# Kernel tuning notes

Measured on AMD Instinct MI355X. Metric: run time of the kernel, lower is better.

The kernel has to match this reference:

```python
import math
import jax, jax.numpy as jnp
import numpy as np

N, NFEAT, NHID, NCLASS, NLAYERS = 8192, 500, 128, 40, 4
ALPHA, GAMMA, LAMBDA, MAX_W = 0.1, 0.1, 0.5, 0.05


def _col_stochastic(w):
    # Uniform(0,1) -> clamp to [0, MAX_W] -> column normalize (ColumnStochasticGraphConvolution init)
    w = jnp.clip(w, 0.0, MAX_W)
    return w / jnp.clip(w.sum(axis=0, keepdims=True), 1e-8, None)


def setup_inputs() -> dict:
    key = jax.random.key(0)
    ks = jax.random.split(key, 10)
    x = jax.random.normal(ks[0], (N, NFEAT), dtype=jnp.float32)
    adj = (jax.random.uniform(ks[1], (N, N)) < 0.002).astype(jnp.float32)
    s_in = 1.0 / math.sqrt(NFEAT)
    fc_in_w = jax.random.uniform(ks[2], (NFEAT, NHID), minval=-s_in, maxval=s_in, dtype=jnp.float32)
    fc_in_b = jnp.zeros((NHID,), jnp.float32)
    c = jax.random.normal(ks[3], (NHID,), dtype=jnp.float32)
    s_h = 1.0 / math.sqrt(NHID)
    w_gcnii = jax.random.uniform(ks[4], (NLAYERS, NHID, NHID), minval=-s_h, maxval=s_h, dtype=jnp.float32)
    b_gcnii = jax.random.uniform(ks[5], (NLAYERS, NHID), minval=-s_h, maxval=s_h, dtype=jnp.float32)
    w_lin = jax.vmap(_col_stochastic)(jax.random.uniform(ks[6], (NLAYERS, NHID, NHID), dtype=jnp.float32))
    b_lin = jnp.zeros((NLAYERS, NHID), jnp.float32)
    fc_out_w = jax.random.uniform(ks[7], (NHID, NCLASS), minval=-s_h, maxval=s_h, dtype=jnp.float32)
    fc_out_b = jnp.zeros((NCLASS,), jnp.float32)
    return {"x": x, "adj": adj, "fc_in_w": fc_in_w, "fc_in_b": fc_in_b, "c": c,
            "w_gcnii": w_gcnii, "b_gcnii": b_gcnii, "w_lin": w_lin, "b_lin": b_lin,
            "fc_out_w": fc_out_w, "fc_out_b": fc_out_b}


def _normalize_adj(adj):
    # A_hat = D^{-1/2} (A + I) D^{-1/2}
    a = adj + jnp.eye(adj.shape[0], dtype=adj.dtype)
    deg = a.sum(axis=1)
    dinv = jnp.where(deg > 0, jax.lax.rsqrt(deg), 0.0)
    return dinv[:, None] * a * dinv[None, :]


def reference(x, adj, fc_in_w, fc_in_b, c, w_gcnii, b_gcnii, w_lin, b_lin, fc_out_w, fc_out_b):
    a_hat = _normalize_adj(adj)                      # [N, N]
    h = jax.nn.relu(x @ fc_in_w + fc_in_b)           # [N, nhid]
    h = (1.0 - GAMMA) * h + GAMMA * c[None, :]       # H0 preconditioning with learnable c
    h0 = h
    # dropout is identity in eval mode
    for i in range(NLAYERS):
        beta = math.log(LAMBDA / (i + 1) + 1.0)
        # linear propagation branch: A_hat @ (H W'_i) + b'_i  (column-stochastic W')
        linear_part = a_hat @ (h @ w_lin[i]) + b_lin[i]
        # GCNII branch: sigma(((1-a) A_hat H + a H0)((1-b) I + b W_i)) + b_i
        support = (1.0 - ALPHA) * (a_hat @ h) + ALPHA * h0
        gcnii = jax.nn.relu((1.0 - beta) * support + beta * (support @ w_gcnii[i]) + b_gcnii[i])
        h = linear_part + gcnii
    return h @ fc_out_w + fc_out_b                   # [N, nclass] logits
```

## Files before the change

### kernel.cpp

```cpp
#include <hip/hip_runtime.h>
#include <math.h>

#define NROWS 8192
#define NFEATD 500
#define NHID 128
#define NCLS 40
#define CAP 64
#define FCIN_BLOCKS (NROWS / 8)
#define CSR_BLOCKS  (NROWS / 4)

typedef float f32x4 __attribute__((ext_vector_type(4)));

__global__ __launch_bounds__(256) void k_pre(
    const float* __restrict__ x, const float* __restrict__ w,
    const float* __restrict__ b, const float* __restrict__ c,
    const float* __restrict__ adj,
    float* __restrict__ h, float* __restrict__ h0,
    float* __restrict__ dinv, int* __restrict__ cnts, int* __restrict__ cols)
{
    __shared__ float xs[8][504];
    int tid = threadIdx.x;
    if (blockIdx.x < FCIN_BLOCKS) {
        int col = tid & 127;
        int rg = tid >> 7;
        int r0 = blockIdx.x * 8;
        for (int rr = 0; rr < 8; ++rr)
            for (int k = tid; k < NFEATD; k += 256)
                xs[rr][k] = x[(size_t)(r0 + rr) * NFEATD + k];
        __syncthreads();
        float bias = b[col];
        float acc[4] = {bias, bias, bias, bias};
        for (int k4 = 0; k4 < NFEATD / 4; ++k4) {
            int k = k4 * 4;
            f32x4 a0 = *(const f32x4*)&xs[rg * 4 + 0][k];
            f32x4 a1 = *(const f32x4*)&xs[rg * 4 + 1][k];
            f32x4 a2 = *(const f32x4*)&xs[rg * 4 + 2][k];
            f32x4 a3 = *(const f32x4*)&xs[rg * 4 + 3][k];
            float w0 = w[(k + 0) * NHID + col];
            float w1 = w[(k + 1) * NHID + col];
            float w2 = w[(k + 2) * NHID + col];
            float w3 = w[(k + 3) * NHID + col];
            acc[0] += a0.x * w0 + a0.y * w1 + a0.z * w2 + a0.w * w3;
            acc[1] += a1.x * w0 + a1.y * w1 + a1.z * w2 + a1.w * w3;
            acc[2] += a2.x * w0 + a2.y * w1 + a2.z * w2 + a2.w * w3;
            acc[3] += a3.x * w0 + a3.y * w1 + a3.z * w2 + a3.w * w3;
        }
        float cv = c[col];
#pragma unroll
        for (int rr = 0; rr < 4; ++rr) {
            float hv = 0.9f * fmaxf(acc[rr], 0.0f) + 0.1f * cv;
            size_t o = (size_t)(r0 + rg * 4 + rr) * NHID + col;
            h[o] = hv;
            h0[o] = hv;
        }
    } else {
        int bid = blockIdx.x - FCIN_BLOCKS;
        int r = bid * 4 + (tid >> 6);
        int lane = tid & 63;
        const f32x4* row4 = (const f32x4*)(adj + (size_t)r * NROWS);
        int* mycols = cols + (size_t)r * CAP;
        unsigned long long lt = (1ull << lane) - 1ull;
        int cnt = 0;
        for (int it = 0; it < NROWS / 256; ++it) {
            f32x4 v = __builtin_nontemporal_load(&row4[it * 64 + lane]);
            int base = it * 256 + 4 * lane;
            bool nz; unsigned long long m;
            nz = (v.x != 0.0f); m = __ballot(nz);
            if (nz) { int p = cnt + __popcll(m & lt); mycols[p < CAP ? p : CAP - 1] = base; }
            cnt += __popcll(m);
            nz = (v.y != 0.0f); m = __ballot(nz);
            if (nz) { int p = cnt + __popcll(m & lt); mycols[p < CAP ? p : CAP - 1] = base + 1; }
            cnt += __popcll(m);
            nz = (v.z != 0.0f); m = __ballot(nz);
            if (nz) { int p = cnt + __popcll(m & lt); mycols[p < CAP ? p : CAP - 1] = base + 2; }
            cnt += __popcll(m);
            nz = (v.w != 0.0f); m = __ballot(nz);
            if (nz) { int p = cnt + __popcll(m & lt); mycols[p < CAP ? p : CAP - 1] = base + 3; }
            cnt += __popcll(m);
        }
        if (lane == 0) {
            cnts[r] = cnt < CAP ? cnt : CAP;
            dinv[r] = rsqrtf((float)cnt + 1.0f);
        }
    }
}

__global__ __launch_bounds__(256) void k_layer(
    const float* __restrict__ hin, const float* __restrict__ h0,
    const float* __restrict__ dinv, const int* __restrict__ cnts,
    const int* __restrict__ cols,
    const float* __restrict__ wlin, const float* __restrict__ blin,
    const float* __restrict__ wg, const float* __restrict__ bg,
    float beta, float* __restrict__ hout)
{
    __shared__ float ahs[8][NHID];
    __shared__ float ss[8][NHID];
    int tid = threadIdx.x;
    int lane = tid & 63;
    int wid = tid >> 6;
    int r0 = blockIdx.x * 8;

    for (int rr = 2 * wid; rr < 2 * wid + 2; ++rr) {
        int r = r0 + rr;
        int n = cnts[r];
        const int* mc = cols + (size_t)r * CAP;
        float ax = 0.f, ay = 0.f;
        int e = 0;
        for (; e + 4 <= n; e += 4) {
            int j0 = mc[e], j1 = mc[e + 1], j2 = mc[e + 2], j3 = mc[e + 3];
            float d0 = dinv[j0], d1 = dinv[j1], d2 = dinv[j2], d3 = dinv[j3];
            float2 v0 = ((const float2*)(hin + (size_t)j0 * NHID))[lane];
            float2 v1 = ((const float2*)(hin + (size_t)j1 * NHID))[lane];
            float2 v2 = ((const float2*)(hin + (size_t)j2 * NHID))[lane];
            float2 v3 = ((const float2*)(hin + (size_t)j3 * NHID))[lane];
            ax += d0 * v0.x + d1 * v1.x + d2 * v2.x + d3 * v3.x;
            ay += d0 * v0.y + d1 * v1.y + d2 * v2.y + d3 * v3.y;
        }
        for (; e < n; ++e) {
            int j = mc[e];
            float dj = dinv[j];
            float2 v = ((const float2*)(hin + (size_t)j * NHID))[lane];
            ax += dj * v.x;
            ay += dj * v.y;
        }
        float di = dinv[r];
        float2 vi = ((const float2*)(hin + (size_t)r * NHID))[lane];
        ax = di * (ax + di * vi.x);
        ay = di * (ay + di * vi.y);
        float2 h0v = ((const float2*)(h0 + (size_t)r * NHID))[lane];
        ((float2*)&ahs[rr][0])[lane] = make_float2(ax, ay);
        ((float2*)&ss[rr][0])[lane] =
            make_float2(0.9f * ax + 0.1f * h0v.x, 0.9f * ay + 0.1f * h0v.y);
    }
    __syncthreads();

    int col = tid & 127;
    int rg = tid >> 7;
    float accl[4] = {0, 0, 0, 0};
    float accg[4] = {0, 0, 0, 0};
    for (int k4 = 0; k4 < NHID / 4; ++k4) {
        int k = k4 * 4;
        f32x4 a0 = *(const f32x4*)&ahs[rg * 4 + 0][k];
        f32x4 a1 = *(const f32x4*)&ahs[rg * 4 + 1][k];
        f32x4 a2 = *(const f32x4*)&ahs[rg * 4 + 2][k];
        f32x4 a3 = *(const f32x4*)&ahs[rg * 4 + 3][k];
        f32x4 s0 = *(const f32x4*)&ss[rg * 4 + 0][k];
        f32x4 s1 = *(const f32x4*)&ss[rg * 4 + 1][k];
        f32x4 s2 = *(const f32x4*)&ss[rg * 4 + 2][k];
        f32x4 s3 = *(const f32x4*)&ss[rg * 4 + 3][k];
        float wl0 = wlin[(k + 0) * NHID + col];
        float wl1 = wlin[(k + 1) * NHID + col];
        float wl2 = wlin[(k + 2) * NHID + col];
        float wl3 = wlin[(k + 3) * NHID + col];
        float wg0 = wg[(k + 0) * NHID + col];
        float wg1 = wg[(k + 1) * NHID + col];
        float wg2 = wg[(k + 2) * NHID + col];
        float wg3 = wg[(k + 3) * NHID + col];
        accl[0] += a0.x * wl0 + a0.y * wl1 + a0.z * wl2 + a0.w * wl3;
        accl[1] += a1.x * wl0 + a1.y * wl1 + a1.z * wl2 + a1.w * wl3;
        accl[2] += a2.x * wl0 + a2.y * wl1 + a2.z * wl2 + a2.w * wl3;
        accl[3] += a3.x * wl0 + a3.y * wl1 + a3.z * wl2 + a3.w * wl3;
        accg[0] += s0.x * wg0 + s0.y * wg1 + s0.z * wg2 + s0.w * wg3;
        accg[1] += s1.x * wg0 + s1.y * wg1 + s1.z * wg2 + s1.w * wg3;
        accg[2] += s2.x * wg0 + s2.y * wg1 + s2.z * wg2 + s2.w * wg3;
        accg[3] += s3.x * wg0 + s3.y * wg1 + s3.z * wg2 + s3.w * wg3;
    }
    float blv = blin[col], bgv = bg[col], omb = 1.0f - beta;
#pragma unroll
    for (int rr = 0; rr < 4; ++rr) {
        int row = r0 + rg * 4 + rr;
        float sv = ss[rg * 4 + rr][col];
        float g = fmaxf(omb * sv + beta * accg[rr] + bgv, 0.0f);
        hout[(size_t)row * NHID + col] = accl[rr] + blv + g;
    }
}

__global__ void k_fcout(const float* __restrict__ h, const float* __restrict__ w,
                        const float* __restrict__ b, float* __restrict__ out) {
    __shared__ float hs[4][NHID];
    int tid = threadIdx.x;
    int rr = tid >> 6, col = tid & 63;
    int r0 = blockIdx.x * 4;
    for (int idx = tid; idx < 4 * NHID; idx += 256)
        hs[idx >> 7][idx & 127] = h[(size_t)r0 * NHID + idx];
    __syncthreads();
    if (col < NCLS) {
        float acc = b[col];
        for (int k = 0; k < NHID; ++k) acc += hs[rr][k] * w[k * NCLS + col];
        out[(size_t)(r0 + rr) * NCLS + col] = acc;
    }
}

extern "C" void kernel_launch(void* const* d_in, const int* in_sizes, int n_in,
                              void* d_out, int out_size, void* d_ws, size_t ws_size,
                              hipStream_t stream) {
    const float* x        = (const float*)d_in[0];
    const float* adj      = (const float*)d_in[1];
    const float* fc_in_w  = (const float*)d_in[2];
    const float* fc_in_b  = (const float*)d_in[3];
    const float* c        = (const float*)d_in[4];
    const float* w_gcnii  = (const float*)d_in[5];
    const float* b_gcnii  = (const float*)d_in[6];
    const float* w_lin    = (const float*)d_in[7];
    const float* b_lin    = (const float*)d_in[8];
    const float* fc_out_w = (const float*)d_in[9];
    const float* fc_out_b = (const float*)d_in[10];
    float* out = (float*)d_out;

    char* ws = (char*)d_ws;
    size_t off = 0;
    auto alloc = [&](size_t bytes) -> void* {
        void* p = ws + off;
        off += (bytes + 255) & ~(size_t)255;
        return p;
    };
    float* dinv = (float*)alloc((size_t)NROWS * 4);
    int*   cnts = (int*)  alloc((size_t)NROWS * 4);
    int*   cols = (int*)  alloc((size_t)NROWS * CAP * 4);
    float* hA   = (float*)alloc((size_t)NROWS * NHID * 4);
    float* hB   = (float*)alloc((size_t)NROWS * NHID * 4);
    float* h0   = (float*)alloc((size_t)NROWS * NHID * 4);

    k_pre<<<FCIN_BLOCKS + CSR_BLOCKS, 256, 0, stream>>>(
        x, fc_in_w, fc_in_b, c, adj, hA, h0, dinv, cnts, cols);

    float* bufs[2] = {hA, hB};
    for (int i = 0; i < 4; ++i) {
        float beta = logf(0.5f / (float)(i + 1) + 1.0f);
        k_layer<<<NROWS / 8, 256, 0, stream>>>(
            bufs[i & 1], h0, dinv, cnts, cols,
            w_lin + (size_t)i * NHID * NHID, b_lin + (size_t)i * NHID,
            w_gcnii + (size_t)i * NHID * NHID, b_gcnii + (size_t)i * NHID,
            beta, bufs[(i + 1) & 1]);
    }
    k_fcout<<<NROWS / 4, 256, 0, stream>>>(bufs[0], fc_out_w, fc_out_b, out);
}
```

Measured before the change: 211.1 us.

## Interleave four rows per wave in gather and vectorize weight GEMM

```diff
diff --git a/kernel.cpp b/kernel.cpp
--- a/kernel.cpp
+++ b/kernel.cpp
@@ -8,8 +8,16 @@
 #define CAP 64
 #define FCIN_BLOCKS (NROWS / 8)
 #define CSR_BLOCKS  (NROWS / 4)
+#define ROWS_PB 16
 
 typedef float f32x4 __attribute__((ext_vector_type(4)));
+
+__device__ __forceinline__ f32x4 relu4(f32x4 v) {
+    f32x4 r;
+    r.x = fmaxf(v.x, 0.f); r.y = fmaxf(v.y, 0.f);
+    r.z = fmaxf(v.z, 0.f); r.w = fmaxf(v.w, 0.f);
+    return r;
+}
 
 __global__ __launch_bounds__(256) void k_pre(
     const float* __restrict__ x, const float* __restrict__ w,
@@ -93,86 +101,94 @@
     const float* __restrict__ wg, const float* __restrict__ bg,
     float beta, float* __restrict__ hout)
 {
-    __shared__ float ahs[8][NHID];
-    __shared__ float ss[8][NHID];
+    __shared__ float ahs[ROWS_PB][NHID];
+    __shared__ float ss[ROWS_PB][NHID];
     int tid = threadIdx.x;
     int lane = tid & 63;
     int wid = tid >> 6;
-    int r0 = blockIdx.x * 8;
-
-    for (int rr = 2 * wid; rr < 2 * wid + 2; ++rr) {
-        int r = r0 + rr;
-        int n = cnts[r];
-        const int* mc = cols + (size_t)r * CAP;
-        float ax = 0.f, ay = 0.f;
-        int e = 0;
-        for (; e + 4 <= n; e += 4) {
-            int j0 = mc[e], j1 = mc[e + 1], j2 = mc[e + 2], j3 = mc[e + 3];
-            float d0 = dinv[j0], d1 = dinv[j1], d2 = dinv[j2], d3 = dinv[j3];
-            float2 v0 = ((const float2*)(hin + (size_t)j0 * NHID))[lane];
-            float2 v1 = ((const float2*)(hin + (size_t)j1 * NHID))[lane];
-            float2 v2 = ((const float2*)(hin + (size_t)j2 * NHID))[lane];
-            float2 v3 = ((const float2*)(hin + (size_t)j3 * NHID))[lane];
-            ax += d0 * v0.x + d1 * v1.x + d2 * v2.x + d3 * v3.x;
-            ay += d0 * v0.y + d1 * v1.y + d2 * v2.y + d3 * v3.y;
-        }
-        for (; e < n; ++e) {
-            int j = mc[e];
-            float dj = dinv[j];
-            float2 v = ((const float2*)(hin + (size_t)j * NHID))[lane];
-            ax += dj * v.x;
-            ay += dj * v.y;
-        }
-        float di = dinv[r];
-        float2 vi = ((const float2*)(hin + (size_t)r * NHID))[lane];
-        ax = di * (ax + di * vi.x);
-        ay = di * (ay + di * vi.y);
-        float2 h0v = ((const float2*)(h0 + (size_t)r * NHID))[lane];
-        ((float2*)&ahs[rr][0])[lane] = make_float2(ax, ay);
-        ((float2*)&ss[rr][0])[lane] =
-            make_float2(0.9f * ax + 0.1f * h0v.x, 0.9f * ay + 0.1f * h0v.y);
+    int r0 = blockIdx.x * ROWS_PB;
+    const float2* h2 = (const float2*)hin;
+    const float2* h02 = (const float2*)h0;
+
+    {
+        int rb = r0 + wid * 4;
+        float ax[4] = {0.f, 0.f, 0.f, 0.f};
+        float ay[4] = {0.f, 0.f, 0.f, 0.f};
+        int n[4];
+        const int* mc[4];
+#pragma unroll
+        for (int rr = 0; rr < 4; ++rr) {
+            n[rr] = cnts[rb + rr];
+            mc[rr] = cols + (size_t)(rb + rr) * CAP;
+        }
+        int nmax = max(max(n[0], n[1]), max(n[2], n[3]));
+        for (int e = 0; e < nmax; e += 2) {
+#pragma unroll
+            for (int rr = 0; rr < 4; ++rr) {
+#pragma unroll
+                for (int u = 0; u < 2; ++u) {
+                    int ee = e + u;
+                    int cl = ee < n[rr] ? ee : (n[rr] > 0 ? n[rr] - 1 : 0);
+                    int j = mc[rr][cl] & (NROWS - 1);
+                    float dj = ee < n[rr] ? dinv[j] : 0.f;
+                    float2 v = h2[(size_t)j * 64 + lane];
+                    ax[rr] += dj * v.x;
+                    ay[rr] += dj * v.y;
+                }
+            }
+        }
+#pragma unroll
+        for (int rr = 0; rr < 4; ++rr) {
+            int r = rb + rr;
+            int lr = wid * 4 + rr;
+            float di = dinv[r];
+            float2 vi = h2[(size_t)r * 64 + lane];
+            float gx = di * (ax[rr] + di * vi.x);
+            float gy = di * (ay[rr] + di * vi.y);
+            float2 h0v = h02[(size_t)r * 64 + lane];
+            ((float2*)&ahs[lr][0])[lane] = make_float2(gx, gy);
+            ((float2*)&ss[lr][0])[lane] =
+                make_float2(0.9f * gx + 0.1f * h0v.x, 0.9f * gy + 0.1f * h0v.y);
+        }
     }
     __syncthreads();
 
-    int col = tid & 127;
-    int rg = tid >> 7;
-    float accl[4] = {0, 0, 0, 0};
-    float accg[4] = {0, 0, 0, 0};
+    int cp = tid & 31;
+    int rg = tid >> 5;
+    const float* wlc = wlin + 4 * cp;
+    const float* wgc = wg + 4 * cp;
+    f32x4 accl0 = {0, 0, 0, 0}, accl1 = {0, 0, 0, 0};
+    f32x4 accg0 = {0, 0, 0, 0}, accg1 = {0, 0, 0, 0};
     for (int k4 = 0; k4 < NHID / 4; ++k4) {
-        int k = k4 * 4;
-        f32x4 a0 = *(const f32x4*)&ahs[rg * 4 + 0][k];
-        f32x4 a1 = *(const f32x4*)&ahs[rg * 4 + 1][k];
-        f32x4 a2 = *(const f32x4*)&ahs[rg * 4 + 2][k];
-        f32x4 a3 = *(const f32x4*)&ahs[rg * 4 + 3][k];
-        f32x4 s0 = *(const f32x4*)&ss[rg * 4 + 0][k];
-        f32x4 s1 = *(const f32x4*)&ss[rg * 4 + 1][k];
-        f32x4 s2 = *(const f32x4*)&ss[rg * 4 + 2][k];
-        f32x4 s3 = *(const f32x4*)&ss[rg * 4 + 3][k];
-        float wl0 = wlin[(k + 0) * NHID + col];
-        float wl1 = wlin[(k + 1) * NHID + col];
-        float wl2 = wlin[(k + 2) * NHID + col];
-        float wl3 = wlin[(k + 3) * NHID + col];
-        float wg0 = wg[(k + 0) * NHID + col];
-        float wg1 = wg[(k + 1) * NHID + col];
-        float wg2 = wg[(k + 2) * NHID + col];
-        float wg3 = wg[(k + 3) * NHID + col];
-        accl[0] += a0.x * wl0 + a0.y * wl1 + a0.z * wl2 + a0.w * wl3;
-        accl[1] += a1.x * wl0 + a1.y * wl1 + a1.z * wl2 + a1.w * wl3;
-        accl[2] += a2.x * wl0 + a2.y * wl1 + a2.z * wl2 + a2.w * wl3;
-        accl[3] += a3.x * wl0 + a3.y * wl1 + a3.z * wl2 + a3.w * wl3;
-        accg[0] += s0.x * wg0 + s0.y * wg1 + s0.z * wg2 + s0.w * wg3;
-        accg[1] += s1.x * wg0 + s1.y * wg1 + s1.z * wg2 + s1.w * wg3;
-        accg[2] += s2.x * wg0 + s2.y * wg1 + s2.z * wg2 + s2.w * wg3;
-        accg[3] += s3.x * wg0 + s3.y * wg1 + s3.z * wg2 + s3.w * wg3;
-    }
-    float blv = blin[col], bgv = bg[col], omb = 1.0f - beta;
-#pragma unroll
-    for (int rr = 0; rr < 4; ++rr) {
-        int row = r0 + rg * 4 + rr;
-        float sv = ss[rg * 4 + rr][col];
-        float g = fmaxf(omb * sv + beta * accg[rr] + bgv, 0.0f);
-        hout[(size_t)row * NHID + col] = accl[rr] + blv + g;
-    }
+        int k = 4 * k4;
+        f32x4 a0 = *(const f32x4*)&ahs[2 * rg][k];
+        f32x4 a1 = *(const f32x4*)&ahs[2 * rg + 1][k];
+        f32x4 s0 = *(const f32x4*)&ss[2 * rg][k];
+        f32x4 s1 = *(const f32x4*)&ss[2 * rg + 1][k];
+        f32x4 wl0 = *(const f32x4*)&wlc[(size_t)(k + 0) * NHID];
+        f32x4 wl1 = *(const f32x4*)&wlc[(size_t)(k + 1) * NHID];
+        f32x4 wl2 = *(const f32x4*)&wlc[(size_t)(k + 2) * NHID];
+        f32x4 wl3 = *(const f32x4*)&wlc[(size_t)(k + 3) * NHID];
+        f32x4 wg0 = *(const f32x4*)&wgc[(size_t)(k + 0) * NHID];
+        f32x4 wg1 = *(const f32x4*)&wgc[(size_t)(k + 1) * NHID];
+        f32x4 wg2 = *(const f32x4*)&wgc[(size_t)(k + 2) * NHID];
+        f32x4 wg3 = *(const f32x4*)&wgc[(size_t)(k + 3) * NHID];
+        accl0 += a0.x * wl0 + a0.y * wl1 + a0.z * wl2 + a0.w * wl3;
+        accl1 += a1.x * wl0 + a1.y * wl1 + a1.z * wl2 + a1.w * wl3;
+        accg0 += s0.x * wg0 + s0.y * wg1 + s0.z * wg2 + s0.w * wg3;
+        accg1 += s1.x * wg0 + s1.y * wg1 + s1.z * wg2 + s1.w * wg3;
+    }
+    f32x4 blv = *(const f32x4*)&blin[4 * cp];
+    f32x4 bgv = *(const f32x4*)&bg[4 * cp];
+    float omb = 1.0f - beta;
+    f32x4 sv0 = *(const f32x4*)&ss[2 * rg][4 * cp];
+    f32x4 sv1 = *(const f32x4*)&ss[2 * rg + 1][4 * cp];
+    f32x4 g0 = relu4(omb * sv0 + beta * accg0 + bgv);
+    f32x4 g1 = relu4(omb * sv1 + beta * accg1 + bgv);
+    f32x4 o0 = accl0 + blv + g0;
+    f32x4 o1 = accl1 + blv + g1;
+    *(f32x4*)&hout[(size_t)(r0 + 2 * rg) * NHID + 4 * cp] = o0;
+    *(f32x4*)&hout[(size_t)(r0 + 2 * rg + 1) * NHID + 4 * cp] = o1;
 }
 
 __global__ void k_fcout(const float* __restrict__ h, const float* __restrict__ w,
@@ -227,7 +243,7 @@
     float* bufs[2] = {hA, hB};
     for (int i = 0; i < 4; ++i) {
         float beta = logf(0.5f / (float)(i + 1) + 1.0f);
-        k_layer<<<NROWS / 8, 256, 0, stream>>>(
+        k_layer<<<NROWS / ROWS_PB, 256, 0, stream>>>(
             bufs[i & 1], h0, dinv, cnts, cols,
             w_lin + (size_t)i * NHID * NHID, b_lin + (size_t)i * NHID,
             w_gcnii + (size_t)i * NHID * NHID, b_gcnii + (size_t)i * NHID,
```

New measurement: 344.1 us. 1.63x slower.

## Pre-scale hidden rows by dinv and fuse output projection into last layer

Applied to the files above, without the earlier changes.

```diff
diff --git a/kernel.cpp b/kernel.cpp
--- a/kernel.cpp
+++ b/kernel.cpp
@@ -8,6 +8,7 @@
 #define CAP 64
 #define FCIN_BLOCKS (NROWS / 8)
 #define CSR_BLOCKS  (NROWS / 4)
+#define ROWS_PB 8
 
 typedef float f32x4 __attribute__((ext_vector_type(4)));
 
@@ -85,20 +86,34 @@
     }
 }
 
+__global__ __launch_bounds__(256) void k_scale(
+    const float* __restrict__ h, const float* __restrict__ dinv,
+    float* __restrict__ ht)
+{
+    int gid = blockIdx.x * 256 + threadIdx.x;
+    float2 v = ((const float2*)h)[gid];
+    float d = dinv[gid >> 6];
+    ((float2*)ht)[gid] = make_float2(v.x * d, v.y * d);
+}
+
 __global__ __launch_bounds__(256) void k_layer(
-    const float* __restrict__ hin, const float* __restrict__ h0,
+    const float* __restrict__ ht, const float* __restrict__ h0,
     const float* __restrict__ dinv, const int* __restrict__ cnts,
     const int* __restrict__ cols,
     const float* __restrict__ wlin, const float* __restrict__ blin,
     const float* __restrict__ wg, const float* __restrict__ bg,
-    float beta, float* __restrict__ hout)
+    float beta, float* __restrict__ htout,
+    const float* __restrict__ fow, const float* __restrict__ fob,
+    float* __restrict__ out, int final_layer)
 {
-    __shared__ float ahs[8][NHID];
-    __shared__ float ss[8][NHID];
+    __shared__ float ahs[ROWS_PB][NHID];
+    __shared__ float ss[ROWS_PB][NHID];
     int tid = threadIdx.x;
     int lane = tid & 63;
     int wid = tid >> 6;
-    int r0 = blockIdx.x * 8;
+    int r0 = blockIdx.x * ROWS_PB;
+    const float2* ht2 = (const float2*)ht;
+    const float2* h02 = (const float2*)h0;
 
     for (int rr = 2 * wid; rr < 2 * wid + 2; ++rr) {
         int r = r0 + rr;
@@ -108,29 +123,27 @@
         int e = 0;
         for (; e + 4 <= n; e += 4) {
             int j0 = mc[e], j1 = mc[e + 1], j2 = mc[e + 2], j3 = mc[e + 3];
-            float d0 = dinv[j0], d1 = dinv[j1], d2 = dinv[j2], d3 = dinv[j3];
-            float2 v0 = ((const float2*)(hin + (size_t)j0 * NHID))[lane];
-            float2 v1 = ((const float2*)(hin + (size_t)j1 * NHID))[lane];
-            float2 v2 = ((const float2*)(hin + (size_t)j2 * NHID))[lane];
-            float2 v3 = ((const float2*)(hin + (size_t)j3 * NHID))[lane];
-            ax += d0 * v0.x + d1 * v1.x + d2 * v2.x + d3 * v3.x;
-            ay += d0 * v0.y + d1 * v1.y + d2 * v2.y + d3 * v3.y;
+            float2 v0 = ht2[(size_t)j0 * 64 + lane];
+            float2 v1 = ht2[(size_t)j1 * 64 + lane];
+            float2 v2 = ht2[(size_t)j2 * 64 + lane];
+            float2 v3 = ht2[(size_t)j3 * 64 + lane];
+            ax += v0.x + v1.x + v2.x + v3.x;
+            ay += v0.y + v1.y + v2.y + v3.y;
         }
         for (; e < n; ++e) {
             int j = mc[e];
-            float dj = dinv[j];
-            float2 v = ((const float2*)(hin + (size_t)j * NHID))[lane];
-            ax += dj * v.x;
-            ay += dj * v.y;
+            float2 v = ht2[(size_t)j * 64 + lane];
+            ax += v.x;
+            ay += v.y;
         }
         float di = dinv[r];
-        float2 vi = ((const float2*)(hin + (size_t)r * NHID))[lane];
-        ax = di * (ax + di * vi.x);
-        ay = di * (ay + di * vi.y);
-        float2 h0v = ((const float2*)(h0 + (size_t)r * NHID))[lane];
-        ((float2*)&ahs[rr][0])[lane] = make_float2(ax, ay);
+        float2 ti = ht2[(size_t)r * 64 + lane];
+        float gx = di * (ax + ti.x);
+        float gy = di * (ay + ti.y);
+        float2 h0v = h02[(size_t)r * 64 + lane];
+        ((float2*)&ahs[rr][0])[lane] = make_float2(gx, gy);
         ((float2*)&ss[rr][0])[lane] =
-            make_float2(0.9f * ax + 0.1f * h0v.x, 0.9f * ay + 0.1f * h0v.y);
+            make_float2(0.9f * gx + 0.1f * h0v.x, 0.9f * gy + 0.1f * h0v.y);
     }
     __syncthreads();
 
@@ -139,7 +152,7 @@
     float accl[4] = {0, 0, 0, 0};
     float accg[4] = {0, 0, 0, 0};
     for (int k4 = 0; k4 < NHID / 4; ++k4) {
-        int k = k4 * 4;
+        int k = 4 * k4;
         f32x4 a0 = *(const f32x4*)&ahs[rg * 4 + 0][k];
         f32x4 a1 = *(const f32x4*)&ahs[rg * 4 + 1][k];
         f32x4 a2 = *(const f32x4*)&ahs[rg * 4 + 2][k];
@@ -165,29 +178,39 @@
         accg[2] += s2.x * wg0 + s2.y * wg1 + s2.z * wg2 + s2.w * wg3;
         accg[3] += s3.x * wg0 + s3.y * wg1 + s3.z * wg2 + s3.w * wg3;
     }
-    float blv = blin[col], bgv = bg[col], omb = 1.0f - beta;
+    float blv = blin[col], bgv = bg[col];
+    float omb = 1.0f - beta;
+    float o[4];
 #pragma unroll
     for (int rr = 0; rr < 4; ++rr) {
-        int row = r0 + rg * 4 + rr;
         float sv = ss[rg * 4 + rr][col];
         float g = fmaxf(omb * sv + beta * accg[rr] + bgv, 0.0f);
-        hout[(size_t)row * NHID + col] = accl[rr] + blv + g;
-    }
-}
-
-__global__ void k_fcout(const float* __restrict__ h, const float* __restrict__ w,
-                        const float* __restrict__ b, float* __restrict__ out) {
-    __shared__ float hs[4][NHID];
-    int tid = threadIdx.x;
-    int rr = tid >> 6, col = tid & 63;
-    int r0 = blockIdx.x * 4;
-    for (int idx = tid; idx < 4 * NHID; idx += 256)
-        hs[idx >> 7][idx & 127] = h[(size_t)r0 * NHID + idx];
-    __syncthreads();
-    if (col < NCLS) {
-        float acc = b[col];
-        for (int k = 0; k < NHID; ++k) acc += hs[rr][k] * w[k * NCLS + col];
-        out[(size_t)(r0 + rr) * NCLS + col] = acc;
+        o[rr] = accl[rr] + blv + g;
+    }
+
+    if (!final_layer) {
+#pragma unroll
+        for (int rr = 0; rr < 4; ++rr) {
+            int row = r0 + rg * 4 + rr;
+            htout[(size_t)row * NHID + col] = dinv[row] * o[rr];
+        }
+    } else {
+        __syncthreads();
+#pragma unroll
+        for (int rr = 0; rr < 4; ++rr)
+            ahs[rg * 4 + rr][col] = o[rr];
+        __syncthreads();
+        int rr2 = tid >> 6, c2 = tid & 63;
+        if (c2 < NCLS) {
+#pragma unroll
+            for (int half = 0; half < 2; ++half) {
+                int lr = half * 4 + rr2;
+                float acc = fob[c2];
+                for (int k = 0; k < NHID; ++k)
+                    acc += ahs[lr][k] * fow[k * NCLS + c2];
+                out[(size_t)(r0 + lr) * NCLS + c2] = acc;
+            }
+        }
     }
 }
 
@@ -218,20 +241,22 @@
     int*   cnts = (int*)  alloc((size_t)NROWS * 4);
     int*   cols = (int*)  alloc((size_t)NROWS * CAP * 4);
     float* hA   = (float*)alloc((size_t)NROWS * NHID * 4);
-    float* hB   = (float*)alloc((size_t)NROWS * NHID * 4);
     float* h0   = (float*)alloc((size_t)NROWS * NHID * 4);
+    float* htA  = (float*)alloc((size_t)NROWS * NHID * 4);
+    float* htB  = (float*)alloc((size_t)NROWS * NHID * 4);
 
     k_pre<<<FCIN_BLOCKS + CSR_BLOCKS, 256, 0, stream>>>(
         x, fc_in_w, fc_in_b, c, adj, hA, h0, dinv, cnts, cols);
-
-    float* bufs[2] = {hA, hB};
+    k_scale<<<NROWS * 64 / 256, 256, 0, stream>>>(hA, dinv, htA);
+
+    float* htb[2] = {htA, htB};
     for (int i = 0; i < 4; ++i) {
         float beta = logf(0.5f / (float)(i + 1) + 1.0f);
-        k_layer<<<NROWS / 8, 256, 0, stream>>>(
-            bufs[i & 1], h0, dinv, cnts, cols,
+        k_layer<<<NROWS / ROWS_PB, 256, 0, stream>>>(
+            htb[i & 1], h0, dinv, cnts, cols,
             w_lin + (size_t)i * NHID * NHID, b_lin + (size_t)i * NHID,
             w_gcnii + (size_t)i * NHID * NHID, b_gcnii + (size_t)i * NHID,
-            beta, bufs[(i + 1) & 1]);
-    }
-    k_fcout<<<NROWS / 4, 256, 0, stream>>>(bufs[0], fc_out_w, fc_out_b, out);
-}
+            beta, htb[(i + 1) & 1],
+            fc_out_w, fc_out_b, out, (i == 3) ? 1 : 0);
+    }
+}
```

New measurement: 207.9 us. Within noise of the previous version (-1.5%).
